# Kernel optimization log

Hardware: AMD Instinct MI355X
Metric: run time of the kernel (lower is better)

The kernel has to match this reference:

```python
import jax, jax.numpy as jnp
import numpy as np

B, LS, LL = 1024, 128, 2048
E, VOCAB = 16, 160000
NH, KD = 8, 6
LSH_DIM, TOPK = 16, 48
D_ITEM = 3 * E  # 48
EPS = 1e-3  # keras LayerNormalization default epsilon


def setup_inputs() -> dict:
    key = jax.random.key(0)
    ks = iter(jax.random.split(key, 64))
    def nk():
        return next(ks)
    def ids(shape):
        return jax.random.randint(nk(), shape, 0, VOCAB, dtype=jnp.int32)
    inp = {}
    for n in ['uid', 'utag1', 'utag2', 'utag3', 'utag4',
              'label_goods_ids', 'label_shop_ids', 'label_cate_ids']:
        inp[n] = ids((B,))
    for n in ['shortterm_goods_ids', 'shortterm_shop_ids', 'shortterm_cate_ids']:
        inp[n] = ids((B, LS))
    for n in ['longterm_goods_ids', 'longterm_shop_ids', 'longterm_cate_ids']:
        inp[n] = ids((B, LL))
    def rn(shape, s=0.05):
        return (jax.random.normal(nk(), shape) * s).astype(jnp.float32)
    inp['emb_table'] = rn((VOCAB, E))
    inp['H'] = rn((D_ITEM, LSH_DIM), 1.0)  # non-trainable random projection
    for p in ('s', 'l'):
        inp[p + 'Wq'] = rn((D_ITEM, NH, KD)); inp[p + 'bq'] = jnp.zeros((NH, KD), jnp.float32)
        inp[p + 'Wk'] = rn((D_ITEM, NH, KD)); inp[p + 'bk'] = jnp.zeros((NH, KD), jnp.float32)
        inp[p + 'Wv'] = rn((D_ITEM, NH, KD)); inp[p + 'bv'] = jnp.zeros((NH, KD), jnp.float32)
        inp[p + 'Wo'] = rn((NH, KD, D_ITEM)); inp[p + 'bo'] = jnp.zeros((D_ITEM,), jnp.float32)
    Din = D_ITEM + 5 * E + D_ITEM + D_ITEM  # 224
    inp['W1'] = rn((Din, 200)); inp['b1'] = jnp.zeros((200,), jnp.float32)
    inp['g1'] = jnp.ones((200,), jnp.float32); inp['be1'] = jnp.zeros((200,), jnp.float32)
    inp['W2'] = rn((200, 80)); inp['b2'] = jnp.zeros((80,), jnp.float32)
    inp['g2'] = jnp.ones((80,), jnp.float32); inp['be2'] = jnp.zeros((80,), jnp.float32)
    inp['W3'] = rn((80, 1)); inp['b3'] = jnp.zeros((1,), jnp.float32)
    return inp


def _ln(x, g, b):
    m = jnp.mean(x, axis=-1, keepdims=True)
    v = jnp.mean((x - m) ** 2, axis=-1, keepdims=True)
    return (x - m) * jax.lax.rsqrt(v + EPS) * g + b


def _mha(q, kv, mask3, Wq, bq, Wk, bk, Wv, bv, Wo, bo):
    # q: [B,1,D], kv: [B,K,D], mask3: [B,1,K] float (1=keep)
    qh = jnp.einsum('bqe,ehd->bqhd', q, Wq) + bq
    kh = jnp.einsum('bke,ehd->bkhd', kv, Wk) + bk
    vh = jnp.einsum('bke,ehd->bkhd', kv, Wv) + bv
    sc = jnp.einsum('bqhd,bkhd->bhqk', qh, kh) / jnp.sqrt(jnp.float32(KD))
    sc = sc + (1.0 - mask3[:, None, :, :]) * jnp.float32(-1e9)
    a = jax.nn.softmax(sc, axis=-1)
    o = jnp.einsum('bhqk,bkhd->bqhd', a, vh)
    return jnp.einsum('bqhd,hde->bqe', o, Wo) + bo


def reference(uid, utag1, utag2, utag3, utag4,
              label_goods_ids, label_shop_ids, label_cate_ids,
              shortterm_goods_ids, shortterm_shop_ids, shortterm_cate_ids,
              longterm_goods_ids, longterm_shop_ids, longterm_cate_ids,
              emb_table, H,
              sWq, sbq, sWk, sbk, sWv, sbv, sWo, sbo,
              lWq, lbq, lWk, lbk, lWv, lbv, lWo, lbo,
              W1, b1, g1, be1, W2, b2, g2, be2, W3, b3):
    short_mask = shortterm_goods_ids == 0  # padding_index == 0
    long_mask = longterm_goods_ids == 0

    def stack_embed(lst):
        X = jnp.stack([t if t.ndim == 2 else t[:, None] for t in lst], axis=2)  # [B,L,F]
        Xe = emb_table[X]  # [B,L,F,E]
        return Xe.reshape(Xe.shape[0], Xe.shape[1], -1)

    X_item = stack_embed([label_goods_ids, label_shop_ids, label_cate_ids])  # [B,1,48]
    X_user = stack_embed([uid, utag1, utag2, utag3, utag4])                  # [B,1,80]
    X_short = stack_embed([shortterm_goods_ids, shortterm_shop_ids, shortterm_cate_ids])  # [B,LS,48]
    X_long = stack_embed([longterm_goods_ids, longterm_shop_ids, longterm_cate_ids])      # [B,LL,48]

    # short-term interest
    slen = jnp.sum((~short_mask).astype(jnp.int32), axis=1)
    smask = (jnp.arange(LS)[None, :] < slen[:, None]).astype(jnp.float32)[:, None, :]
    short_int = _mha(X_item, X_short, smask, sWq, sbq, sWk, sbk, sWv, sbv, sWo, sbo)[:, 0]

    # long-term interest: LSH sign-hash hamming top-k retrieval
    series_codes = jnp.sign(jnp.einsum('ble,em->blm', X_long, H))  # [B,LL,16]
    item_codes = jnp.sign(jnp.einsum('ble,em->blm', X_item, H))    # [B,1,16]
    scores = jnp.sum((series_codes == item_codes).astype(jnp.float32), axis=-1)  # [B,LL]
    scores = jnp.where(long_mask, -jnp.inf, scores)
    _, idx = jax.lax.top_k(scores, TOPK)  # descending, padded entries last
    top_emb = jnp.take_along_axis(X_long, idx[:, :, None], axis=1)  # [B,TOPK,48]
    top_mask = jnp.take_along_axis(long_mask, idx, axis=1)
    llen = jnp.sum((~top_mask).astype(jnp.int32), axis=1)
    lmask = (jnp.arange(TOPK)[None, :] < llen[:, None]).astype(jnp.float32)[:, None, :]
    long_int = _mha(X_item, top_emb, lmask, lWq, lbq, lWk, lbk, lWv, lbv, lWo, lbo)[:, 0]

    x = jnp.concatenate([X_item[:, 0], X_user[:, 0], short_int, long_int], axis=1)  # [B,224]
    h1 = jax.nn.relu(_ln(x @ W1 + b1, g1, be1))
    h2 = jax.nn.relu(_ln(h1 @ W2 + b2, g2, be2))
    out = jax.nn.sigmoid(h2 @ W3 + b3)  # [B,1]
    return out
```

## Files before the change

kernel.cpp:

```cpp
#include <hip/hip_runtime.h>
#include <math.h>

#define BB 1024
#define LSx 128
#define LLx 2048
#define TOPKx 48

__global__ __launch_bounds__(256, 2) void k_score(
    const int* __restrict__ lg, const int* __restrict__ lsh, const int* __restrict__ lc,
    const int* __restrict__ ig, const int* __restrict__ ish, const int* __restrict__ ici,
    const float* __restrict__ emb, const float* __restrict__ Hm,
    signed char* __restrict__ gsc)
{
  __shared__ float Xitem[48];
  __shared__ int icode[16];
  __shared__ __align__(16) float4 xsh[256][5];
  const int b = blockIdx.y, tid = threadIdx.x;

  const int l = blockIdx.x * 256 + tid;
  const size_t off = (size_t)b * LLx + l;
  const int gid = lg[off];

  if (tid < 48) {
    const int seg = tid >> 4, e = tid & 15;
    const int id = (seg == 0) ? ig[b] : (seg == 1) ? ish[b] : ici[b];
    Xitem[tid] = emb[(size_t)id * 16 + e];
  }
  __syncthreads();
  if (tid < 16) {
    float dd = 0.f;
    for (int e = 0; e < 48; ++e) dd += Xitem[e] * Hm[e * 16 + tid];
    icode[tid] = (dd > 0.f) ? 1 : (dd < 0.f ? -1 : 0);
  }

  const int srow = tid >> 2;
  const int q = tid & 3;
  const size_t bbase = (size_t)b * LLx + (size_t)blockIdx.x * 256;

  float d[16];
  #pragma unroll
  for (int m = 0; m < 16; ++m) d[m] = 0.f;

  #pragma unroll
  for (int seg = 0; seg < 3; ++seg) {
    const int* idarr = (seg == 0) ? lg : (seg == 1) ? lsh : lc;
    #pragma unroll
    for (int jj = 0; jj < 4; ++jj) {
      const int pos = jj * 64 + srow;
      const int id = idarr[bbase + pos];
      xsh[pos][q] = *(const float4*)(emb + (size_t)id * 16 + q * 4);
    }
    __syncthreads();
    if (gid != 0) {
      float x[16];
      #pragma unroll
      for (int qq = 0; qq < 4; ++qq) {
        const float4 r = xsh[tid][qq];
        x[qq * 4 + 0] = r.x; x[qq * 4 + 1] = r.y;
        x[qq * 4 + 2] = r.z; x[qq * 4 + 3] = r.w;
      }
      const float* hb = Hm + seg * 256;
      #pragma unroll
      for (int i = 0; i < 16; ++i) {
        const float xi = x[i];
        #pragma unroll
        for (int mc = 0; mc < 4; ++mc) {
          const float4 h4 = *(const float4*)(hb + i * 16 + mc * 4);
          d[mc * 4 + 0] += xi * h4.x;
          d[mc * 4 + 1] += xi * h4.y;
          d[mc * 4 + 2] += xi * h4.z;
          d[mc * 4 + 3] += xi * h4.w;
        }
      }
    }
    if (seg < 2) __syncthreads();
  }

  int sc = -1;
  if (gid != 0) {
    sc = 0;
    #pragma unroll
    for (int m = 0; m < 16; ++m) {
      const int cs = (d[m] > 0.f) ? 1 : (d[m] < 0.f ? -1 : 0);
      sc += (cs == icode[m]) ? 1 : 0;
    }
  }
  gsc[off] = (signed char)sc;
}

__device__ __forceinline__ float block_sum256(float v, float* red) {
  #pragma unroll
  for (int m = 32; m >= 1; m >>= 1) v += __shfl_xor(v, m, 64);
  const int lane = threadIdx.x & 63, wave = threadIdx.x >> 6;
  if (lane == 0) red[wave] = v;
  __syncthreads();
  const float t = red[0] + red[1] + red[2] + red[3];
  __syncthreads();
  return t;
}

__global__ __launch_bounds__(256) void k_fused(
    const int* __restrict__ sg, const int* __restrict__ ss, const int* __restrict__ scd,
    const int* __restrict__ lg, const int* __restrict__ ls, const int* __restrict__ lcd,
    const int* __restrict__ ig, const int* __restrict__ ish, const int* __restrict__ ici,
    const int* __restrict__ uid, const int* __restrict__ u1, const int* __restrict__ u2,
    const int* __restrict__ u3, const int* __restrict__ u4,
    const float* __restrict__ emb,
    const float* __restrict__ sWq, const float* __restrict__ sbq,
    const float* __restrict__ sWk, const float* __restrict__ sbk,
    const float* __restrict__ sWv, const float* __restrict__ sbv,
    const float* __restrict__ sWo, const float* __restrict__ sbo,
    const float* __restrict__ lWq, const float* __restrict__ lbq,
    const float* __restrict__ lWk, const float* __restrict__ lbk,
    const float* __restrict__ lWv, const float* __restrict__ lbv,
    const float* __restrict__ lWo, const float* __restrict__ lbo,
    const signed char* __restrict__ gsc,
    const float* __restrict__ W1, const float* __restrict__ b1,
    const float* __restrict__ g1, const float* __restrict__ be1,
    const float* __restrict__ W2, const float* __restrict__ b2,
    const float* __restrict__ g2, const float* __restrict__ be2,
    const float* __restrict__ W3, const float* __restrict__ b3,
    float* __restrict__ out)
{
  __shared__ float Xitem[48];
  __shared__ float qh_s[48], qh_l[48];
  __shared__ __align__(16) float vhs_s[LSx][48];
  __shared__ float scs_s[8][LSx + 4];
  __shared__ __align__(16) float vhs_l[TOPKx][48];
  __shared__ float scs_l[8][TOPKx + 4];
  __shared__ float osm_s[48], osm_l[48];
  __shared__ unsigned char validf_s[LSx];
  __shared__ unsigned char validf_l[TOPKx];
  __shared__ int hist[18], wsum[4], nv[4], selsh[TOPKx];
  __shared__ int cnt_above;
  __shared__ __align__(16) float x[224];
  __shared__ __align__(16) float h1[200];
  __shared__ float h2[80];
  __shared__ float red[4];

  const int b = blockIdx.x, tid = threadIdx.x;
  const bool shorth = tid < 128;
  const int t = shorth ? tid : tid - 128;

  const int2 myv = ((const int2*)(gsc + (size_t)b * LLx))[tid];
  signed char loc[8];
  *(int2*)loc = myv;

  if (tid < 48) {
    const int seg = tid >> 4, e = tid & 15;
    const int id = (seg == 0) ? ig[b] : (seg == 1) ? ish[b] : ici[b];
    Xitem[tid] = emb[(size_t)id * 16 + e];
  }
  if (tid >= 160 && tid < 240) {
    const int u = tid - 160;
    const int f = u >> 4;
    const int id = (f == 0) ? uid[b] : (f == 1) ? u1[b] : (f == 2) ? u2[b]
                 : (f == 3) ? u3[b] : u4[b];
    x[48 + u] = emb[(size_t)id * 16 + (u & 15)];
  }
  if (tid < 18) hist[tid] = 0;
  if (tid == 0) cnt_above = 0;
  __syncthreads();

  #pragma unroll
  for (int j = 0; j < 8; ++j) atomicAdd(&hist[(int)loc[j] + 1], 1);
  if (tid < 48) {
    float a = sbq[tid];
    for (int e = 0; e < 48; ++e) a += Xitem[e] * sWq[e * 48 + tid];
    qh_s[tid] = a;
  } else if (tid >= 64 && tid < 112) {
    x[tid - 64] = Xitem[tid - 64];
  } else if (tid >= 128 && tid < 176) {
    float a = lbq[t];
    for (int e = 0; e < 48; ++e) a += Xitem[e] * lWq[e * 48 + t];
    qh_l[t] = a;
  }
  __syncthreads();

  int above = 0, tval = -1, need = 0;
  for (int s = 16; s >= -1; --s) {
    const int c = hist[s + 1];
    if (above + c >= TOPKx) { tval = s; need = TOPKx - above; break; }
    above += c;
  }
  const int base_l = tid * (LLx / 256);
  int cnt = 0;
  #pragma unroll
  for (int j = 0; j < 8; ++j) cnt += ((int)loc[j] == tval) ? 1 : 0;
  int v = cnt;
  const int lane = tid & 63, wave = tid >> 6;
  #pragma unroll
  for (int o = 1; o < 64; o <<= 1) {
    const int u = __shfl_up(v, o, 64);
    if (lane >= o) v += u;
  }
  if (lane == 63) wsum[wave] = v;
  __syncthreads();
  int rank = v - cnt;
  for (int w = 0; w < wave; ++w) rank += wsum[w];

  #pragma unroll
  for (int j = 0; j < 8; ++j) {
    const int l = base_l + j;
    const int s = (int)loc[j];
    if (s > tval) {
      const int slot = atomicAdd(&cnt_above, 1);
      selsh[slot] = l;
    } else if (s == tval) {
      if (rank < need) selsh[above + rank] = l;
      ++rank;
    }
  }
  __syncthreads();

  int gid = 0, sid = 0, cid = 0;
  if (shorth) {
    const size_t off = (size_t)b * LSx + t;
    gid = sg[off]; sid = ss[off]; cid = scd[off];
  } else if (t < TOPKx) {
    const int pos = selsh[t];
    const size_t off = (size_t)b * LLx + pos;
    gid = lg[off]; sid = ls[off]; cid = lcd[off];
  }
  const unsigned long long bal = __ballot(gid != 0);
  if ((tid & 63) == 0) nv[tid >> 6] = __popcll(bal);
  __syncthreads();
  const int nval = shorth ? (nv[0] + nv[1]) : (nv[2] + nv[3]);

  if (shorth) {
    validf_s[t] = (unsigned char)(t < nval);
    float kh[48], vh[48];
    #pragma unroll
    for (int j = 0; j < 48; ++j) { kh[j] = sbk[j]; vh[j] = sbv[j]; }
    const int ids3[3] = {gid, sid, cid};
    #pragma unroll
    for (int seg = 0; seg < 3; ++seg) {
      const float* row = emb + (size_t)ids3[seg] * 16;
      #pragma unroll
      for (int i4 = 0; i4 < 4; ++i4) {
        const float4 xv = ((const float4*)row)[i4];
        const float xs[4] = {xv.x, xv.y, xv.z, xv.w};
        #pragma unroll
        for (int c = 0; c < 4; ++c) {
          const int e = seg * 16 + i4 * 4 + c;
          const float* wkr = sWk + e * 48;
          const float* wvr = sWv + e * 48;
          const float xe = xs[c];
          #pragma unroll
          for (int j = 0; j < 48; ++j) {
            kh[j] += xe * wkr[j];
            vh[j] += xe * wvr[j];
          }
        }
      }
    }
    #pragma unroll
    for (int h = 0; h < 8; ++h) {
      float s = 0.f;
      #pragma unroll
      for (int d = 0; d < 6; ++d) s += qh_s[h * 6 + d] * kh[h * 6 + d];
      scs_s[h][t] = s * 0.40824829046386301637f;
    }
    #pragma unroll
    for (int j = 0; j < 48; ++j) vhs_s[t][j] = vh[j];
  } else if (t < TOPKx) {
    validf_l[t] = (unsigned char)(gid != 0);
    float kh[48], vh[48];
    #pragma unroll
    for (int j = 0; j < 48; ++j) { kh[j] = lbk[j]; vh[j] = lbv[j]; }
    const int ids3[3] = {gid, sid, cid};
    #pragma unroll
    for (int seg = 0; seg < 3; ++seg) {
      const float* row = emb + (size_t)ids3[seg] * 16;
      #pragma unroll
      for (int i4 = 0; i4 < 4; ++i4) {
        const float4 xv = ((const float4*)row)[i4];
        const float xs[4] = {xv.x, xv.y, xv.z, xv.w};
        #pragma unroll
        for (int c = 0; c < 4; ++c) {
          const int e = seg * 16 + i4 * 4 + c;
          const float* wkr = lWk + e * 48;
          const float* wvr = lWv + e * 48;
          const float xe = xs[c];
          #pragma unroll
          for (int j = 0; j < 48; ++j) {
            kh[j] += xe * wkr[j];
            vh[j] += xe * wvr[j];
          }
        }
      }
    }
    #pragma unroll
    for (int h = 0; h < 8; ++h) {
      float s = 0.f;
      #pragma unroll
      for (int d = 0; d < 6; ++d) s += qh_l[h * 6 + d] * kh[h * 6 + d];
      scs_l[h][t] = s * 0.40824829046386301637f;
    }
    #pragma unroll
    for (int j = 0; j < 48; ++j) vhs_l[t][j] = vh[j];
  }
  __syncthreads();

  {
    const int h = t >> 4, l16 = t & 15;
    if (shorth) {
      float amax = -INFINITY;
      for (int k = l16; k < LSx; k += 16) if (validf_s[k]) amax = fmaxf(amax, scs_s[h][k]);
      #pragma unroll
      for (int m = 1; m < 16; m <<= 1) amax = fmaxf(amax, __shfl_xor(amax, m, 16));
      if (nval == 0) {
        for (int k = l16; k < LSx; k += 16) scs_s[h][k] = 1.0f / (float)LSx;
      } else {
        float ssum = 0.f;
        for (int k = l16; k < LSx; k += 16) {
          const float ev = validf_s[k] ? expf(scs_s[h][k] - amax) : 0.f;
          scs_s[h][k] = ev;
          ssum += ev;
        }
        #pragma unroll
        for (int m = 1; m < 16; m <<= 1) ssum += __shfl_xor(ssum, m, 16);
        const float inv = 1.0f / ssum;
        for (int k = l16; k < LSx; k += 16) scs_s[h][k] *= inv;
      }
    } else {
      float amax = -INFINITY;
      for (int k = l16; k < TOPKx; k += 16) if (validf_l[k]) amax = fmaxf(amax, scs_l[h][k]);
      #pragma unroll
      for (int m = 1; m < 16; m <<= 1) amax = fmaxf(amax, __shfl_xor(amax, m, 16));
      if (nval == 0) {
        for (int k = l16; k < TOPKx; k += 16) scs_l[h][k] = 1.0f / (float)TOPKx;
      } else {
        float ssum = 0.f;
        for (int k = l16; k < TOPKx; k += 16) {
          const float ev = validf_l[k] ? expf(scs_l[h][k] - amax) : 0.f;
          scs_l[h][k] = ev;
          ssum += ev;
        }
        #pragma unroll
        for (int m = 1; m < 16; m <<= 1) ssum += __shfl_xor(ssum, m, 16);
        const float inv = 1.0f / ssum;
        for (int k = l16; k < TOPKx; k += 16) scs_l[h][k] *= inv;
      }
    }
  }
  __syncthreads();

  if (tid < 48) {
    const int h = tid / 6;
    float a = 0.f;
    for (int k = 0; k < LSx; ++k) a += scs_s[h][k] * vhs_s[k][tid];
    osm_s[tid] = a;
  } else if (!shorth && t < 48) {
    const int h = t / 6;
    float a = 0.f;
    for (int k = 0; k < TOPKx; ++k) a += scs_l[h][k] * vhs_l[k][t];
    osm_l[t] = a;
  }
  __syncthreads();

  if (tid < 48) {
    float r = sbo[tid];
    for (int j = 0; j < 48; ++j) r += osm_s[j] * sWo[j * 48 + tid];
    x[128 + tid] = r;
  } else if (!shorth && t < 48) {
    float r = lbo[t];
    for (int j = 0; j < 48; ++j) r += osm_l[j] * lWo[j * 48 + t];
    x[176 + t] = r;
  }
  __syncthreads();

  float v1 = 0.f;
  if (tid < 200) {
    v1 = b1[tid];
    for (int i4 = 0; i4 < 56; ++i4) {
      const float4 xv = *(const float4*)(x + i4 * 4);
      const float* w = W1 + i4 * 4 * 200 + tid;
      v1 += xv.x * w[0];
      v1 += xv.y * w[200];
      v1 += xv.z * w[400];
      v1 += xv.w * w[600];
    }
  }
  const float mean1 = block_sum256((tid < 200) ? v1 : 0.f, red) * (1.0f / 200.0f);
  const float dv = (tid < 200) ? (v1 - mean1) : 0.f;
  const float var1 = block_sum256(dv * dv, red) * (1.0f / 200.0f);
  if (tid < 200) {
    const float y = (v1 - mean1) * rsqrtf(var1 + 1e-3f) * g1[tid] + be1[tid];
    h1[tid] = fmaxf(y, 0.f);
  }
  __syncthreads();

  float v2 = 0.f;
  if (tid < 80) {
    v2 = b2[tid];
    for (int i4 = 0; i4 < 50; ++i4) {
      const float4 xv = *(const float4*)(h1 + i4 * 4);
      const float* w = W2 + i4 * 4 * 80 + tid;
      v2 += xv.x * w[0];
      v2 += xv.y * w[80];
      v2 += xv.z * w[160];
      v2 += xv.w * w[240];
    }
  }
  const float mean2 = block_sum256((tid < 80) ? v2 : 0.f, red) * (1.0f / 80.0f);
  const float dv2 = (tid < 80) ? (v2 - mean2) : 0.f;
  const float var2 = block_sum256(dv2 * dv2, red) * (1.0f / 80.0f);
  if (tid < 80) {
    const float y = (v2 - mean2) * rsqrtf(var2 + 1e-3f) * g2[tid] + be2[tid];
    h2[tid] = fmaxf(y, 0.f);
  }
  __syncthreads();

  const float p = (tid < 80) ? h2[tid] * W3[tid] : 0.f;
  const float z = block_sum256(p, red);
  if (tid == 0) {
    out[b] = 1.0f / (1.0f + expf(-(z + b3[0])));
  }
}

extern "C" void kernel_launch(void* const* d_in, const int* in_sizes, int n_in,
                              void* d_out, int out_size, void* d_ws, size_t ws_size,
                              hipStream_t stream) {
  (void)in_sizes; (void)n_in; (void)out_size; (void)ws_size;
  const int* uid = (const int*)d_in[0];
  const int* u1  = (const int*)d_in[1];
  const int* u2  = (const int*)d_in[2];
  const int* u3  = (const int*)d_in[3];
  const int* u4  = (const int*)d_in[4];
  const int* ig  = (const int*)d_in[5];
  const int* ish = (const int*)d_in[6];
  const int* ici = (const int*)d_in[7];
  const int* sg  = (const int*)d_in[8];
  const int* ss  = (const int*)d_in[9];
  const int* scd = (const int*)d_in[10];
  const int* lg  = (const int*)d_in[11];
  const int* ls  = (const int*)d_in[12];
  const int* lcd = (const int*)d_in[13];
  const float* emb = (const float*)d_in[14];
  const float* Hm  = (const float*)d_in[15];
  const float* sWq = (const float*)d_in[16];
  const float* sbq = (const float*)d_in[17];
  const float* sWk = (const float*)d_in[18];
  const float* sbk = (const float*)d_in[19];
  const float* sWv = (const float*)d_in[20];
  const float* sbv = (const float*)d_in[21];
  const float* sWo = (const float*)d_in[22];
  const float* sbo = (const float*)d_in[23];
  const float* lWq = (const float*)d_in[24];
  const float* lbq = (const float*)d_in[25];
  const float* lWk = (const float*)d_in[26];
  const float* lbk = (const float*)d_in[27];
  const float* lWv = (const float*)d_in[28];
  const float* lbv = (const float*)d_in[29];
  const float* lWo = (const float*)d_in[30];
  const float* lbo = (const float*)d_in[31];
  const float* W1 = (const float*)d_in[32];
  const float* b1 = (const float*)d_in[33];
  const float* g1 = (const float*)d_in[34];
  const float* be1 = (const float*)d_in[35];
  const float* W2 = (const float*)d_in[36];
  const float* b2 = (const float*)d_in[37];
  const float* g2 = (const float*)d_in[38];
  const float* be2 = (const float*)d_in[39];
  const float* W3 = (const float*)d_in[40];
  const float* b3 = (const float*)d_in[41];
  float* out = (float*)d_out;

  signed char* gsc = (signed char*)d_ws;

  k_score<<<dim3(LLx / 256, BB), dim3(256), 0, stream>>>(
      lg, ls, lcd, ig, ish, ici, emb, Hm, gsc);
  k_fused<<<dim3(BB), dim3(256), 0, stream>>>(
      sg, ss, scd, lg, ls, lcd, ig, ish, ici,
      uid, u1, u2, u3, u4, emb,
      sWq, sbq, sWk, sbk, sWv, sbv, sWo, sbo,
      lWq, lbq, lWk, lbk, lWv, lbv, lWo, lbo,
      gsc,
      W1, b1, g1, be1, W2, b2, g2, be2, W3, b3, out);
}
```

Baseline: 332.2 us.

## Shrink fused-kernel LDS with transposed two-phase V buffer and two-block occupancy

Adds a min-blocks hint of 2 to the fused kernel and cuts the short-term value buffer from 128x48 to a transposed 48x65 tile. The value buffer is filled in two halves, with an extra barrier phase between them, so the 48 output threads accumulate over keys 0-63 and then 64-127. The long-term value buffer is also transposed with padding, which changes the LDS bank-access pattern. This aims to fit two blocks per CU, at the cost of extra barriers and keeping vh live in registers across phases, which may spill under the tighter register limit.

```diff
diff --git a/kernel.cpp b/kernel.cpp
--- a/kernel.cpp
+++ b/kernel.cpp
@@ -99,7 +99,7 @@
   return t;
 }
 
-__global__ __launch_bounds__(256) void k_fused(
+__global__ __launch_bounds__(256, 2) void k_fused(
     const int* __restrict__ sg, const int* __restrict__ ss, const int* __restrict__ scd,
     const int* __restrict__ lg, const int* __restrict__ ls, const int* __restrict__ lcd,
     const int* __restrict__ ig, const int* __restrict__ ish, const int* __restrict__ ici,
@@ -124,9 +124,9 @@
 {
   __shared__ float Xitem[48];
   __shared__ float qh_s[48], qh_l[48];
-  __shared__ __align__(16) float vhs_s[LSx][48];
+  __shared__ float vhs_sT[48][65];
   __shared__ float scs_s[8][LSx + 4];
-  __shared__ __align__(16) float vhs_l[TOPKx][48];
+  __shared__ float vhs_lT[48][TOPKx + 1];
   __shared__ float scs_l[8][TOPKx + 4];
   __shared__ float osm_s[48], osm_l[48];
   __shared__ unsigned char validf_s[LSx];
@@ -227,9 +227,10 @@
   __syncthreads();
   const int nval = shorth ? (nv[0] + nv[1]) : (nv[2] + nv[3]);
 
+  float vh[48];
   if (shorth) {
     validf_s[t] = (unsigned char)(t < nval);
-    float kh[48], vh[48];
+    float kh[48];
     #pragma unroll
     for (int j = 0; j < 48; ++j) { kh[j] = sbk[j]; vh[j] = sbv[j]; }
     const int ids3[3] = {gid, sid, cid};
@@ -261,11 +262,13 @@
       for (int d = 0; d < 6; ++d) s += qh_s[h * 6 + d] * kh[h * 6 + d];
       scs_s[h][t] = s * 0.40824829046386301637f;
     }
-    #pragma unroll
-    for (int j = 0; j < 48; ++j) vhs_s[t][j] = vh[j];
+    if (t < 64) {
+      #pragma unroll
+      for (int j = 0; j < 48; ++j) vhs_sT[j][t] = vh[j];
+    }
   } else if (t < TOPKx) {
     validf_l[t] = (unsigned char)(gid != 0);
-    float kh[48], vh[48];
+    float kh[48];
     #pragma unroll
     for (int j = 0; j < 48; ++j) { kh[j] = lbk[j]; vh[j] = lbv[j]; }
     const int ids3[3] = {gid, sid, cid};
@@ -298,7 +301,7 @@
       scs_l[h][t] = s * 0.40824829046386301637f;
     }
     #pragma unroll
-    for (int j = 0; j < 48; ++j) vhs_l[t][j] = vh[j];
+    for (int j = 0; j < 48; ++j) vhs_lT[j][t] = vh[j];
   }
   __syncthreads();
 
@@ -346,16 +349,28 @@
   }
   __syncthreads();
 
-  if (tid < 48) {
-    const int h = tid / 6;
-    float a = 0.f;
-    for (int k = 0; k < LSx; ++k) a += scs_s[h][k] * vhs_s[k][tid];
-    osm_s[tid] = a;
+  float acc = 0.f;
+  int hh = 0;
+  if (tid < 48) {
+    hh = tid / 6;
+    for (int k = 0; k < 64; ++k) acc += scs_s[hh][k] * vhs_sT[tid][k];
   } else if (!shorth && t < 48) {
     const int h = t / 6;
     float a = 0.f;
-    for (int k = 0; k < TOPKx; ++k) a += scs_l[h][k] * vhs_l[k][t];
+    for (int k = 0; k < TOPKx; ++k) a += scs_l[h][k] * vhs_lT[t][k];
     osm_l[t] = a;
+  }
+  __syncthreads();
+
+  if (shorth && t >= 64) {
+    #pragma unroll
+    for (int j = 0; j < 48; ++j) vhs_sT[j][t - 64] = vh[j];
+  }
+  __syncthreads();
+
+  if (tid < 48) {
+    for (int k = 64; k < LSx; ++k) acc += scs_s[hh][k] * vhs_sT[tid][k - 64];
+    osm_s[tid] = acc;
   }
   __syncthreads();
 
```

New measurement: 328.2 us. Within noise of the previous version (-1.2%).
